# Performance work log

Hardware: AMD Instinct MI355X
Metric: run time of the kernel (lower is better)

The kernel has to match this reference:

```python
import jax, jax.numpy as jnp
import numpy as np

N = 50000
E = 800000
G = 64  # number of graphs in each batch
IN_DIM = 128
HID = 64
NEG_SLOPE = 0.2


def _glorot(key, shape):
    fan = shape[0] + shape[-1] if len(shape) == 2 else int(np.prod(shape[1:])) + shape[-1]
    lim = float(np.sqrt(6.0 / fan))
    return jax.random.uniform(key, shape, jnp.float32, -lim, lim)


def setup_inputs() -> dict:
    key = jax.random.key(0)
    ks = jax.random.split(key, 16)
    x1 = jax.random.normal(ks[0], (N, IN_DIM), jnp.float32)
    x2 = jax.random.normal(ks[1], (N, IN_DIM), jnp.float32)
    edge_index1 = jax.random.randint(ks[2], (2, E), 0, N, jnp.int64)
    edge_index2 = jax.random.randint(ks[3], (2, E), 0, N, jnp.int64)
    batch1 = jnp.sort(jax.random.randint(ks[4], (N,), 0, G, jnp.int64))
    batch2 = jnp.sort(jax.random.randint(ks[5], (N,), 0, G, jnp.int64))
    # conv1: GATConv(IN_DIM, HID, heads=4)
    W1 = _glorot(ks[6], (IN_DIM, 4 * HID))
    a_src1 = _glorot(ks[7], (1, 4, HID))
    a_dst1 = _glorot(ks[8], (1, 4, HID))
    b1 = jnp.zeros((4 * HID,), jnp.float32)
    # conv2: GATConv(4*HID, HID, heads=1)
    W2 = _glorot(ks[9], (4 * HID, HID))
    a_src2 = _glorot(ks[10], (1, 1, HID))
    a_dst2 = _glorot(ks[11], (1, 1, HID))
    b2 = jnp.zeros((HID,), jnp.float32)
    return {"x1": x1, "edge_index1": edge_index1, "batch1": batch1,
            "x2": x2, "edge_index2": edge_index2, "batch2": batch2,
            "W1": W1, "a_src1": a_src1, "a_dst1": a_dst1, "b1": b1,
            "W2": W2, "a_src2": a_src2, "a_dst2": a_dst2, "b2": b2}


def gat_conv(x, src, dst, W, a_src, a_dst, b, n_nodes, heads, out_dim):
    """PyG GATConv with add_self_loops=True, negative_slope=0.2, concat=True."""
    h = (x @ W).reshape(n_nodes, heads, out_dim)            # [N,H,D]
    alpha_s = jnp.sum(h * a_src, axis=-1)                   # [N,H]
    alpha_d = jnp.sum(h * a_dst, axis=-1)                   # [N,H]
    e = alpha_s[src] + alpha_d[dst]                         # [E',H]
    e = jax.nn.leaky_relu(e, NEG_SLOPE)
    # segment softmax over incoming edges of each destination node
    e_max = jax.ops.segment_max(e, dst, num_segments=n_nodes)
    ex = jnp.exp(e - e_max[dst])
    denom = jax.ops.segment_sum(ex, dst, num_segments=n_nodes)
    alpha = ex / (denom[dst] + 1e-16)                       # [E',H]
    msg = h[src] * alpha[:, :, None]                        # [E',H,D]
    out = jax.ops.segment_sum(msg, dst, num_segments=n_nodes)
    return out.reshape(n_nodes, heads * out_dim) + b


def embed(x, edge_index, batch, W1, a_src1, a_dst1, b1, W2, a_src2, a_dst2, b2):
    loops = jnp.arange(N, dtype=edge_index.dtype)
    src = jnp.concatenate([edge_index[0], loops])
    dst = jnp.concatenate([edge_index[1], loops])
    h = jax.nn.elu(gat_conv(x, src, dst, W1, a_src1, a_dst1, b1, N, 4, HID))
    h = jax.nn.elu(gat_conv(h, src, dst, W2, a_src2, a_dst2, b2, N, 1, HID))
    # global_mean_pool over graph ids
    sums = jax.ops.segment_sum(h, batch, num_segments=G)
    cnt = jax.ops.segment_sum(jnp.ones((N,), h.dtype), batch, num_segments=G)
    return sums / jnp.maximum(cnt, 1.0)[:, None]


def reference(x1, edge_index1, batch1, x2, edge_index2, batch2,
              W1, a_src1, a_dst1, b1, W2, a_src2, a_dst2, b2):
    emb1 = embed(x1, edge_index1, batch1, W1, a_src1, a_dst1, b1, W2, a_src2, a_dst2, b2)
    emb2 = embed(x2, edge_index2, batch2, W1, a_src1, a_dst1, b1, W2, a_src2, a_dst2, b2)
    return (emb1, emb2)
```

## Files before the change

### kernel.cpp

```cpp
#include <hip/hip_runtime.h>
#include <cstdint>
#include <cstddef>

#define NNODES 50000
#define NEDGES 800000
#define NGR    64
#define INDIM  128
#define HIDD   64

typedef __attribute__((ext_vector_type(8))) _Float16 f16x8;
typedef __attribute__((ext_vector_type(2))) _Float16 half2v;
typedef __attribute__((ext_vector_type(4))) float f32x4;

__device__ __forceinline__ float lrelu(float x) { return x > 0.f ? x : 0.2f * x; }
__device__ __forceinline__ float eluf(float x)  { return x > 0.f ? x : expm1f(x); }
__device__ __forceinline__ unsigned short f2h(float x) {
    _Float16 h = (_Float16)x;
    return __builtin_bit_cast(unsigned short, h);
}
__device__ __forceinline__ float h2lo(unsigned int u) {
    half2v h = __builtin_bit_cast(half2v, u);
    return (float)h.x;
}
__device__ __forceinline__ float h2hi(unsigned int u) {
    half2v h = __builtin_bit_cast(half2v, u);
    return (float)h.y;
}

__device__ __forceinline__ void acc8(uint4 u, float we, float* a) {
    a[0] = fmaf(h2lo(u.x), we, a[0]); a[1] = fmaf(h2hi(u.x), we, a[1]);
    a[2] = fmaf(h2lo(u.y), we, a[2]); a[3] = fmaf(h2hi(u.y), we, a[3]);
    a[4] = fmaf(h2lo(u.z), we, a[4]); a[5] = fmaf(h2hi(u.z), we, a[5]);
    a[6] = fmaf(h2lo(u.w), we, a[6]); a[7] = fmaf(h2hi(u.w), we, a[7]);
}

__global__ void cvt_f2h(const float* __restrict__ in, unsigned short* __restrict__ out, int n4) {
    int i = blockIdx.x * 256 + threadIdx.x;
    if (i < n4) {
        float4 v = ((const float4*)in)[i];
        ushort4 o;
        o.x = f2h(v.x); o.y = f2h(v.y); o.z = f2h(v.z); o.w = f2h(v.w);
        ((ushort4*)out)[i] = o;
    }
}

__global__ void count_dst(const int* __restrict__ ei0, const int* __restrict__ ei1,
                          int* __restrict__ cnt, int E, int N) {
    const int* ei = blockIdx.y ? ei1 : ei0;
    int* c = cnt + blockIdx.y * N;
    int e = blockIdx.x * 256 + threadIdx.x;
    if (e < E) atomicAdd(&c[ei[E + e]], 1);
}

__global__ __launch_bounds__(256) void scan_part(const int* __restrict__ cnt,
                                                 int* __restrict__ psum, int n) {
    __shared__ int ws[4];
    const int* c = cnt + blockIdx.y * n;
    int* p = psum + blockIdx.y * 256;
    int lane = threadIdx.x & 63, w = threadIdx.x >> 6;
    int i = blockIdx.x * 256 + threadIdx.x;
    int v = (i < n) ? c[i] : 0;
    #pragma unroll
    for (int off = 32; off >= 1; off >>= 1) v += __shfl_xor(v, off, 64);
    if (lane == 0) ws[w] = v;
    __syncthreads();
    if (threadIdx.x == 0) p[blockIdx.x] = ws[0] + ws[1] + ws[2] + ws[3];
}

__global__ __launch_bounds__(256) void scan_tops(int* __restrict__ psum,
                                                 int* __restrict__ rp, int nb, int n) {
    __shared__ int wsum[4];
    int* p = psum + blockIdx.x * 256;
    int* r = rp + blockIdx.x * (n + 1);
    int tid = threadIdx.x, lane = tid & 63, w = tid >> 6;
    int v = (tid < nb) ? p[tid] : 0;
    int x = v;
    #pragma unroll
    for (int off = 1; off < 64; off <<= 1) {
        int t = __shfl_up(x, off, 64);
        if (lane >= off) x += t;
    }
    if (lane == 63) wsum[w] = x;
    __syncthreads();
    int add = 0;
    for (int k = 0; k < w; k++) add += wsum[k];
    int incl = x + add;
    if (tid < nb) p[tid] = incl - v;
    if (tid == nb - 1) r[n] = incl;
}

__global__ __launch_bounds__(256) void scan_fin(const int* __restrict__ cnt,
                                                const int* __restrict__ psum,
                                                int* __restrict__ rp, int n) {
    __shared__ int wsum[4];
    const int* c = cnt + blockIdx.y * n;
    const int* p = psum + blockIdx.y * 256;
    int* r = rp + blockIdx.y * (n + 1);
    int tid = threadIdx.x, lane = tid & 63, w = tid >> 6;
    int i = blockIdx.x * 256 + tid;
    int v = (i < n) ? c[i] : 0;
    int x = v;
    #pragma unroll
    for (int off = 1; off < 64; off <<= 1) {
        int t = __shfl_up(x, off, 64);
        if (lane >= off) x += t;
    }
    if (lane == 63) wsum[w] = x;
    __syncthreads();
    int add = p[blockIdx.x];
    for (int k = 0; k < w; k++) add += wsum[k];
    if (i < n) r[i] = x + add - v;
}

__global__ void fill_csr(const int* __restrict__ ei0, const int* __restrict__ ei1,
                         const int* __restrict__ rp, int* __restrict__ fc,
                         int* __restrict__ col, int E, int N) {
    int g = blockIdx.y;
    const int* ei = g ? ei1 : ei0;
    const int* r = rp + g * (N + 1);
    int* f = fc + g * N;
    int* cl = col + (size_t)g * E;
    int e = blockIdx.x * 256 + threadIdx.x;
    if (e < E) {
        int s = ei[e];
        int d = ei[E + e];
        int pos = atomicAdd(&f[d], 1);
        cl[r[d] + pos] = s;
    }
}

template<int BN, int WM, int WN, bool AF32>
__global__ __launch_bounds__(256) void gemm_mfma(const void* __restrict__ A0,
                                                 const void* __restrict__ A1,
                                                 size_t Ags,
                                                 const unsigned short* __restrict__ Bw,
                                                 unsigned short* __restrict__ C,
                                                 size_t Cgs,
                                                 int M, int K, int N,
                                                 const float* __restrict__ a_src,
                                                 const float* __restrict__ a_dst,
                                                 float* __restrict__ as_o,
                                                 float* __restrict__ ad_o,
                                                 int hstride, int ags) {
    constexpr int BM = 128, BK = 64;
    constexpr int MI = WM / 16, NI = WN / 16;
    constexpr int LDA = BK + 8;
    __shared__ unsigned short Asm[BM * LDA];
    __shared__ unsigned short Bsm[BN * LDA];
    int gph = blockIdx.z;
    const float* Af = (const float*)(gph ? A1 : A0);
    const unsigned short* Ab = (const unsigned short*)A0 + (size_t)gph * Ags;
    unsigned short* Cg = C + (size_t)gph * Cgs;
    float* aso = as_o + (size_t)gph * ags;
    float* ado = ad_o + (size_t)gph * ags;
    int tid = threadIdx.x;
    int lane = tid & 63, wave = tid >> 6;
    int l15 = lane & 15, quad = lane >> 4;
    int wm0, wn0;
    if (BN == 128) { wm0 = (wave >> 1) * 64; wn0 = (wave & 1) * 64; }
    else           { wm0 = wave * 32;        wn0 = 0; }
    int row0 = blockIdx.x * BM;
    int c0 = blockIdx.y * BN;

    f32x4 acc[MI][NI];
    #pragma unroll
    for (int mi = 0; mi < MI; mi++)
        #pragma unroll
        for (int ni = 0; ni < NI; ni++)
            acc[mi][ni] = (f32x4){0.f, 0.f, 0.f, 0.f};

    for (int k0 = 0; k0 < K; k0 += BK) {
        #pragma unroll
        for (int q = 0; q < BM / 32; q++) {
            int idx = q * 256 + tid;
            int r = idx >> 3, kc = idx & 7;
            int row = row0 + r;
            if (AF32) {
                float4 v0 = make_float4(0.f, 0.f, 0.f, 0.f), v1 = v0;
                if (row < M) {
                    v0 = *(const float4*)(Af + (size_t)row * K + k0 + kc * 8);
                    v1 = *(const float4*)(Af + (size_t)row * K + k0 + kc * 8 + 4);
                }
                unsigned short t[8] = {f2h(v0.x), f2h(v0.y), f2h(v0.z), f2h(v0.w),
                                       f2h(v1.x), f2h(v1.y), f2h(v1.z), f2h(v1.w)};
                *(uint4*)&Asm[r * LDA + kc * 8] = *(uint4*)t;
            } else {
                uint4 v = make_uint4(0u, 0u, 0u, 0u);
                if (row < M) v = *(const uint4*)(Ab + (size_t)row * K + k0 + kc * 8);
                *(uint4*)&Asm[r * LDA + kc * 8] = v;
            }
        }
        #pragma unroll
        for (int q = 0; q < BN / 32; q++) {
            int idx = q * 256 + tid;
            int n  = idx & (BN - 1);
            int kc = idx / BN;
            unsigned short tmp[8];
            #pragma unroll
            for (int j = 0; j < 8; j++)
                tmp[j] = Bw[(size_t)(k0 + kc * 8 + j) * N + c0 + n];
            *(uint4*)&Bsm[n * LDA + kc * 8] = *(uint4*)tmp;
        }
        __syncthreads();
        #pragma unroll
        for (int kb = 0; kb < 2; kb++) {
            f16x8 af[MI], bfr[NI];
            #pragma unroll
            for (int mi = 0; mi < MI; mi++)
                af[mi] = *(f16x8*)&Asm[(wm0 + mi * 16 + l15) * LDA + kb * 32 + quad * 8];
            #pragma unroll
            for (int ni = 0; ni < NI; ni++)
                bfr[ni] = *(f16x8*)&Bsm[(wn0 + ni * 16 + l15) * LDA + kb * 32 + quad * 8];
            #pragma unroll
            for (int mi = 0; mi < MI; mi++)
                #pragma unroll
                for (int ni = 0; ni < NI; ni++)
                    acc[mi][ni] = __builtin_amdgcn_mfma_f32_16x16x32_f16(
                        af[mi], bfr[ni], acc[mi][ni], 0, 0, 0);
        }
        __syncthreads();
    }
    #pragma unroll
    for (int mi = 0; mi < MI; mi++) {
        #pragma unroll
        for (int r = 0; r < 4; r++) {
            int row = row0 + wm0 + mi * 16 + quad * 4 + r;
            if (row < M) {
                #pragma unroll
                for (int ni = 0; ni < NI; ni++) {
                    int colg = c0 + wn0 + ni * 16 + l15;
                    Cg[(size_t)row * N + colg] = f2h(acc[mi][ni][r]);
                }
            }
        }
    }
    int headc = (c0 + wn0) >> 6;
    float a_s[NI], a_d[NI];
    #pragma unroll
    for (int ni = 0; ni < NI; ni++) {
        a_s[ni] = a_src[headc * 64 + ni * 16 + l15];
        a_d[ni] = a_dst[headc * 64 + ni * 16 + l15];
    }
    #pragma unroll
    for (int mi = 0; mi < MI; mi++) {
        #pragma unroll
        for (int r = 0; r < 4; r++) {
            float ps = 0.f, pd = 0.f;
            #pragma unroll
            for (int ni = 0; ni < NI; ni++) {
                ps += acc[mi][ni][r] * a_s[ni];
                pd += acc[mi][ni][r] * a_d[ni];
            }
            #pragma unroll
            for (int off = 1; off < 16; off <<= 1) {
                ps += __shfl_xor(ps, off, 64);
                pd += __shfl_xor(pd, off, 64);
            }
            int row = row0 + wm0 + mi * 16 + quad * 4 + r;
            if (l15 == 0 && row < M) {
                aso[row * hstride + headc] = ps;
                ado[row * hstride + headc] = pd;
            }
        }
    }
}

__global__ __launch_bounds__(256) void agg_h4(const unsigned short* __restrict__ h,
                                              size_t hgs,
                                              const float* __restrict__ as_,
                                              const float* __restrict__ ad_, int ags,
                                              const int* __restrict__ rp,
                                              const int* __restrict__ col,
                                              const float* __restrict__ bias,
                                              unsigned short* __restrict__ out,
                                              size_t ogs, int n, int E) {
    int gph = blockIdx.y;
    const uint4* h4 = (const uint4*)(h + (size_t)gph * hgs);
    const float* as = as_ + (size_t)gph * ags;
    const float* adp = ad_ + (size_t)gph * ags;
    const int* r = rp + gph * (n + 1);
    const int* cl = col + (size_t)gph * E;
    unsigned short* og = out + (size_t)gph * ogs;

    int wave = threadIdx.x >> 6, lane = threadIdx.x & 63;
    int node = blockIdx.x * 4 + wave;
    if (node >= n) return;
    int p = lane >> 4;
    int c = lane & 15;
    int headc = c >> 2;
    float adv_q = adp[node * 4 + p];
    float w0 = __expf(lrelu(as[node * 4 + headc] + adp[node * 4 + headc]));
    float m0 = (p == 0) ? w0 : 0.f;
    uint4 hu0 = h4[(size_t)node * 32 + 2 * c];
    uint4 hu1 = h4[(size_t)node * 32 + 2 * c + 1];
    float den = m0;
    float a[16] = {0.f, 0.f, 0.f, 0.f, 0.f, 0.f, 0.f, 0.f,
                   0.f, 0.f, 0.f, 0.f, 0.f, 0.f, 0.f, 0.f};
    acc8(hu0, m0, a);
    acc8(hu1, m0, a + 8);
    int beg = __builtin_amdgcn_readfirstlane(r[node]);
    int end = __builtin_amdgcn_readfirstlane(r[node + 1]);
    int hbase = headc << 4;
    int j = beg;
    int m = end - j; if (m > 16) m = 16;
    int colv = 0; float asv = 0.f;
    if (j < end) {
        colv = cl[j + (c < m ? c : m - 1)];
        asv = as[colv * 4 + p];
    }
    while (j < end) {
        int jn = j + 16;
        int mn = end - jn; if (mn > 16) mn = 16;
        int colv_n = 0; float asv_n = 0.f;
        if (mn > 0) {
            colv_n = cl[jn + (c < mn ? c : mn - 1)];
            asv_n = as[colv_n * 4 + p];
        }
        float wl = __expf(lrelu(asv + adv_q));
        int e0 = p;
        int ec = e0 < m ? e0 : m - 1;
        float we = __shfl(wl, hbase | ec);
        if (e0 >= m) we = 0.f;
        int s = __shfl(colv, ec);
        uint4 u0 = h4[(size_t)s * 32 + 2 * c];
        uint4 u1 = h4[(size_t)s * 32 + 2 * c + 1];
        for (int base = 4; base < m; base += 4) {
            int e2 = base + p;
            int ec2 = e2 < m ? e2 : m - 1;
            float we2 = __shfl(wl, hbase | ec2);
            if (e2 >= m) we2 = 0.f;
            int s2 = __shfl(colv, ec2);
            uint4 v0 = h4[(size_t)s2 * 32 + 2 * c];
            uint4 v1 = h4[(size_t)s2 * 32 + 2 * c + 1];
            den += we;
            acc8(u0, we, a);
            acc8(u1, we, a + 8);
            we = we2; u0 = v0; u1 = v1;
        }
        den += we;
        acc8(u0, we, a);
        acc8(u1, we, a + 8);
        j = jn; m = mn; colv = colv_n; asv = asv_n;
    }
    #pragma unroll
    for (int off = 16; off < 64; off <<= 1) {
        den += __shfl_xor(den, off);
        #pragma unroll
        for (int k = 0; k < 16; k++) a[k] += __shfl_xor(a[k], off);
    }
    if (p == 0) {
        float rden = 1.f / (den + 1e-16f);
        const float4* b4 = (const float4*)bias;
        unsigned short t[16];
        #pragma unroll
        for (int q = 0; q < 4; q++) {
            float4 bq = b4[c * 4 + q];
            t[4 * q]     = f2h(eluf(a[4 * q]     * rden + bq.x));
            t[4 * q + 1] = f2h(eluf(a[4 * q + 1] * rden + bq.y));
            t[4 * q + 2] = f2h(eluf(a[4 * q + 2] * rden + bq.z));
            t[4 * q + 3] = f2h(eluf(a[4 * q + 3] * rden + bq.w));
        }
        uint4* orow = (uint4*)(og + (size_t)node * 256);
        orow[2 * c]     = *(uint4*)&t[0];
        orow[2 * c + 1] = *(uint4*)&t[8];
    }
}

__global__ __launch_bounds__(256) void agg_h1(const unsigned short* __restrict__ h,
                                              size_t hgs,
                                              const float* __restrict__ as_,
                                              const float* __restrict__ ad_,
                                              const int* __restrict__ rp,
                                              const int* __restrict__ col,
                                              const float* __restrict__ bias,
                                              float* __restrict__ out,
                                              size_t ogs, int n, int E) {
    int gph = blockIdx.y;
    const uint4* h4 = (const uint4*)(h + (size_t)gph * hgs);
    const float* as = as_ + (size_t)gph * n;
    const float* adp = ad_ + (size_t)gph * n;
    const int* r = rp + gph * (n + 1);
    const int* cl = col + (size_t)gph * E;
    float* og = out + (size_t)gph * ogs;

    int wave = threadIdx.x >> 6, lane = threadIdx.x & 63;
    int node = blockIdx.x * 4 + wave;
    if (node >= n) return;
    int p = lane >> 3;
    int c = lane & 7;
    float adv = adp[node];
    float w0 = __expf(lrelu(as[node] + adv));
    float m0 = (p == 0) ? w0 : 0.f;
    uint4 hu = h4[(size_t)node * 8 + c];
    float den = m0;
    float a[8] = {0.f, 0.f, 0.f, 0.f, 0.f, 0.f, 0.f, 0.f};
    acc8(hu, m0, a);
    int beg = __builtin_amdgcn_readfirstlane(r[node]);
    int end = __builtin_amdgcn_readfirstlane(r[node + 1]);
    int j = beg;
    int m = end - j; if (m > 64) m = 64;
    int colv = 0; float asv = 0.f;
    if (j < end) {
        colv = cl[j + (lane < m ? lane : m - 1)];
        asv = as[colv];
    }
    while (j < end) {
        int jn = j + 64;
        int mn = end - jn; if (mn > 64) mn = 64;
        int colv_n = 0; float asv_n = 0.f;
        if (mn > 0) {
            colv_n = cl[jn + (lane < mn ? lane : mn - 1)];
            asv_n = as[colv_n];
        }
        float wl = __expf(lrelu(asv + adv));
        int e0 = p;
        int ec = e0 < m ? e0 : m - 1;
        float we = __shfl(wl, ec);
        if (e0 >= m) we = 0.f;
        int s = __shfl(colv, ec);
        uint4 u = h4[(size_t)s * 8 + c];
        for (int base = 8; base < m; base += 8) {
            int e2 = base + p;
            int ec2 = e2 < m ? e2 : m - 1;
            float we2 = __shfl(wl, ec2);
            if (e2 >= m) we2 = 0.f;
            int s2 = __shfl(colv, ec2);
            uint4 u2 = h4[(size_t)s2 * 8 + c];
            den += we;
            acc8(u, we, a);
            we = we2; u = u2;
        }
        den += we;
        acc8(u, we, a);
        j = jn; m = mn; colv = colv_n; asv = asv_n;
    }
    #pragma unroll
    for (int off = 8; off < 64; off <<= 1) {
        den += __shfl_xor(den, off);
        #pragma unroll
        for (int k = 0; k < 8; k++) a[k] += __shfl_xor(a[k], off);
    }
    if (p == 0) {
        float rden = 1.f / (den + 1e-16f);
        float4 b0 = ((const float4*)bias)[c * 2];
        float4 b1 = ((const float4*)bias)[c * 2 + 1];
        float4 o0, o1;
        o0.x = eluf(a[0] * rden + b0.x); o0.y = eluf(a[1] * rden + b0.y);
        o0.z = eluf(a[2] * rden + b0.z); o0.w = eluf(a[3] * rden + b0.w);
        o1.x = eluf(a[4] * rden + b1.x); o1.y = eluf(a[5] * rden + b1.y);
        o1.z = eluf(a[6] * rden + b1.z); o1.w = eluf(a[7] * rden + b1.w);
        float* orow = og + (size_t)node * 64 + c * 8;
        *(float4*)orow = o0;
        *(float4*)(orow + 4) = o1;
    }
}

__device__ __forceinline__ int lbound(const int* __restrict__ a, int n, int key) {
    int lo = 0, hi = n;
    while (lo < hi) {
        int mid = (lo + hi) >> 1;
        if (a[mid] < key) lo = mid + 1; else hi = mid;
    }
    return lo;
}

__global__ __launch_bounds__(256) void pool_mean(const float* __restrict__ g2,
                                                 size_t ggs,
                                                 const int* __restrict__ b0,
                                                 const int* __restrict__ b1,
                                                 float* __restrict__ out, int n) {
    __shared__ float red[4][64];
    __shared__ int bnds[2];
    int gph = blockIdx.y;
    const int* batch = gph ? b1 : b0;
    const float* gg = g2 + (size_t)gph * ggs;
    float* og = out + (size_t)gph * NGR * HIDD;
    int g = blockIdx.x;
    if (threadIdx.x < 2) bnds[threadIdx.x] = lbound(batch, n, g + (int)threadIdx.x);
    __syncthreads();
    int s = bnds[0], e = bnds[1];
    int lane = threadIdx.x & 63, wave = threadIdx.x >> 6;
    float acc = 0.f;
    for (int i = s + wave; i < e; i += 4)
        acc += gg[(size_t)i * 64 + lane];
    red[wave][lane] = acc;
    __syncthreads();
    if (wave == 0) {
        float sum = red[0][lane] + red[1][lane] + red[2][lane] + red[3][lane];
        og[g * 64 + lane] = sum / fmaxf((float)(e - s), 1.0f);
    }
}

extern "C" void kernel_launch(void* const* d_in, const int* in_sizes, int n_in,
                              void* d_out, int out_size, void* d_ws, size_t ws_size,
                              hipStream_t stream) {
    const int N = NNODES, E = NEDGES;

    const float* x1 = (const float*)d_in[0];
    const float* x2 = (const float*)d_in[3];
    const int* ei1v = (const int*)d_in[1];
    const int* ei2v = (const int*)d_in[4];
    const int* ba1  = (const int*)d_in[2];
    const int* ba2  = (const int*)d_in[5];
    const float* W1     = (const float*)d_in[6];
    const float* a_src1 = (const float*)d_in[7];
    const float* a_dst1 = (const float*)d_in[8];
    const float* b1     = (const float*)d_in[9];
    const float* W2     = (const float*)d_in[10];
    const float* a_src2 = (const float*)d_in[11];
    const float* a_dst2 = (const float*)d_in[12];
    const float* b2     = (const float*)d_in[13];

    char* ws = (char*)d_ws;
    size_t off = 0;
    auto carve = [&](size_t bytes) -> char* {
        char* p = ws + off;
        off = (off + bytes + 255) & ~(size_t)255;
        return p;
    };
    char* R1 = carve((size_t)2 * N * 256 * 2);
    char* R2 = carve((size_t)2 * N * 256 * 2);
    char* R3 = carve((size_t)2 * N * 64 * 2);
    int*   col  = (int*)carve((size_t)2 * E * 4);
    int*   rp   = (int*)carve((size_t)2 * (N + 1) * 4);
    int*   cntN = (int*)carve((size_t)2 * N * 4);
    int*   psum = (int*)carve(2 * 256 * 4);
    float* as1  = (float*)carve((size_t)2 * N * 4 * 4);
    float* ad1  = (float*)carve((size_t)2 * N * 4 * 4);
    float* as2  = (float*)carve((size_t)2 * N * 4);
    float* ad2  = (float*)carve((size_t)2 * N * 4);
    unsigned short* W1h = (unsigned short*)carve(INDIM * 256 * 2);
    unsigned short* W2h = (unsigned short*)carve(256 * HIDD * 2);

    unsigned short* h1 = (unsigned short*)R1;
    unsigned short* g1 = (unsigned short*)R2;
    unsigned short* h2 = (unsigned short*)R3;
    float* g2 = (float*)R1;

    float* outF = (float*)d_out;

    const int nodeBlocks = (N + 3) / 4;
    const int nb = (N + 255) / 256;
    const int eb = (E + 255) / 256;

    cvt_f2h<<<(INDIM * 256 / 4 + 255) / 256, 256, 0, stream>>>(W1, W1h, INDIM * 256 / 4);
    cvt_f2h<<<(256 * HIDD / 4 + 255) / 256, 256, 0, stream>>>(W2, W2h, 256 * HIDD / 4);

    hipMemsetAsync(cntN, 0, (size_t)2 * N * 4, stream);
    count_dst<<<dim3(eb, 2), 256, 0, stream>>>(ei1v, ei2v, cntN, E, N);
    scan_part<<<dim3(nb, 2), 256, 0, stream>>>(cntN, psum, N);
    scan_tops<<<2, 256, 0, stream>>>(psum, rp, nb, N);
    scan_fin<<<dim3(nb, 2), 256, 0, stream>>>(cntN, psum, rp, N);
    hipMemsetAsync(cntN, 0, (size_t)2 * N * 4, stream);
    fill_csr<<<dim3(eb, 2), 256, 0, stream>>>(ei1v, ei2v, rp, cntN, col, E, N);

    gemm_mfma<128, 64, 64, true><<<dim3(391, 2, 2), 256, 0, stream>>>(
        x1, x2, 0, W1h, h1, (size_t)N * 256, N, INDIM, 256,
        a_src1, a_dst1, as1, ad1, 4, N * 4);
    agg_h4<<<dim3(nodeBlocks, 2), 256, 0, stream>>>(h1, (size_t)N * 256, as1, ad1, N * 4,
                                                    rp, col, b1, g1, (size_t)N * 256, N, E);

    gemm_mfma<64, 32, 64, false><<<dim3(391, 1, 2), 256, 0, stream>>>(
        g1, nullptr, (size_t)N * 256, W2h, h2, (size_t)N * 64, N, 256, HIDD,
        a_src2, a_dst2, as2, ad2, 1, N);
    agg_h1<<<dim3(nodeBlocks, 2), 256, 0, stream>>>(h2, (size_t)N * 64, as2, ad2,
                                                    rp, col, b2, g2, (size_t)N * 64, N, E);

    pool_mean<<<dim3(NGR, 2), 256, 0, stream>>>(g2, (size_t)N * 64, ba1, ba2, outF, N);
}
```

Baseline: 573.4 us.

## Precompute normalized attention weights, then aggregate with one lane per feature chunk

Splits each GAT aggregation into a weight-prep kernel and an aggregation kernel. The prep kernel computes the softmax-normalized edge weights and stores them as fp16 per edge. The aggregation kernel then walks edges sequentially, with each lane owning a slice of features, so the cross-lane reductions and shuffles of the old version are gone. The cost is two extra kernel launches, a second pass over the edges in prep (exp is computed twice), extra traffic to write and read alpha, and a reuse of the R3 buffer for both alpha1 and h2, which is only safe because of stream ordering.

```diff
diff --git a/kernel.cpp b/kernel.cpp
--- a/kernel.cpp
+++ b/kernel.cpp
@@ -18,6 +18,9 @@
     _Float16 h = (_Float16)x;
     return __builtin_bit_cast(unsigned short, h);
 }
+__device__ __forceinline__ float h2f(unsigned short u) {
+    return (float)__builtin_bit_cast(_Float16, u);
+}
 __device__ __forceinline__ float h2lo(unsigned int u) {
     half2v h = __builtin_bit_cast(half2v, u);
     return (float)h.x;
@@ -25,13 +28,6 @@
 __device__ __forceinline__ float h2hi(unsigned int u) {
     half2v h = __builtin_bit_cast(half2v, u);
     return (float)h.y;
-}
-
-__device__ __forceinline__ void acc8(uint4 u, float we, float* a) {
-    a[0] = fmaf(h2lo(u.x), we, a[0]); a[1] = fmaf(h2hi(u.x), we, a[1]);
-    a[2] = fmaf(h2lo(u.y), we, a[2]); a[3] = fmaf(h2hi(u.y), we, a[3]);
-    a[4] = fmaf(h2lo(u.z), we, a[4]); a[5] = fmaf(h2hi(u.z), we, a[5]);
-    a[6] = fmaf(h2lo(u.w), we, a[6]); a[7] = fmaf(h2hi(u.w), we, a[7]);
 }
 
 __global__ void cvt_f2h(const float* __restrict__ in, unsigned short* __restrict__ out, int n4) {
@@ -265,194 +261,209 @@
     }
 }
 
-__global__ __launch_bounds__(256) void agg_h4(const unsigned short* __restrict__ h,
-                                              size_t hgs,
-                                              const float* __restrict__ as_,
-                                              const float* __restrict__ ad_, int ags,
+__global__ __launch_bounds__(256) void wprep4(const float* __restrict__ as_,
+                                              const float* __restrict__ ad_,
                                               const int* __restrict__ rp,
                                               const int* __restrict__ col,
-                                              const float* __restrict__ bias,
-                                              unsigned short* __restrict__ out,
-                                              size_t ogs, int n, int E) {
+                                              unsigned short* __restrict__ alpha,
+                                              float* __restrict__ alpha0,
+                                              int n, int E) {
     int gph = blockIdx.y;
-    const uint4* h4 = (const uint4*)(h + (size_t)gph * hgs);
-    const float* as = as_ + (size_t)gph * ags;
-    const float* adp = ad_ + (size_t)gph * ags;
+    const float* as = as_ + (size_t)gph * n * 4;
+    const float* ad = ad_ + (size_t)gph * n * 4;
+    const int* r = rp + gph * (n + 1);
+    const int* cl = col + (size_t)gph * E;
+    unsigned short* al = alpha + (size_t)gph * E * 4;
+    float* al0 = alpha0 + (size_t)gph * n * 4;
+
+    int wave = threadIdx.x >> 6, lane = threadIdx.x & 63;
+    int node = blockIdx.x * 4 + wave;
+    if (node >= n) return;
+    int h = lane >> 4, i = lane & 15;
+    float adn = ad[node * 4 + h];
+    float asn = as[node * 4 + h];
+    float w0 = __expf(lrelu(asn + adn));
+    int beg = __builtin_amdgcn_readfirstlane(r[node]);
+    int end = __builtin_amdgcn_readfirstlane(r[node + 1]);
+    float den = 0.f;
+    for (int j = beg; j < end; j += 16) {
+        int idx = j + i;
+        bool v = idx < end;
+        int ix = v ? idx : beg;
+        int colv = cl[ix];
+        float w = __expf(lrelu(as[colv * 4 + h] + adn));
+        den += v ? w : 0.f;
+    }
+    #pragma unroll
+    for (int off = 1; off < 16; off <<= 1) den += __shfl_xor(den, off, 64);
+    den += w0;
+    float rden = 1.f / (den + 1e-16f);
+    for (int j = beg; j < end; j += 16) {
+        int idx = j + i;
+        bool v = idx < end;
+        int ix = v ? idx : beg;
+        int colv = cl[ix];
+        float w = __expf(lrelu(as[colv * 4 + h] + adn));
+        if (v) al[(size_t)idx * 4 + h] = f2h(w * rden);
+    }
+    if (i == 0) al0[node * 4 + h] = w0 * rden;
+}
+
+__global__ __launch_bounds__(256) void wprep1(const float* __restrict__ as_,
+                                              const float* __restrict__ ad_,
+                                              const int* __restrict__ rp,
+                                              const int* __restrict__ col,
+                                              unsigned short* __restrict__ alpha,
+                                              float* __restrict__ alpha0,
+                                              int n, int E) {
+    int gph = blockIdx.y;
+    const float* as = as_ + (size_t)gph * n;
+    const float* ad = ad_ + (size_t)gph * n;
+    const int* r = rp + gph * (n + 1);
+    const int* cl = col + (size_t)gph * E;
+    unsigned short* al = alpha + (size_t)gph * E;
+    float* al0 = alpha0 + (size_t)gph * n;
+
+    int wave = threadIdx.x >> 6, lane = threadIdx.x & 63;
+    int node = blockIdx.x * 4 + wave;
+    if (node >= n) return;
+    float adn = ad[node];
+    float w0 = __expf(lrelu(as[node] + adn));
+    int beg = __builtin_amdgcn_readfirstlane(r[node]);
+    int end = __builtin_amdgcn_readfirstlane(r[node + 1]);
+    float den = 0.f;
+    for (int j = beg; j < end; j += 64) {
+        int idx = j + lane;
+        bool v = idx < end;
+        int ix = v ? idx : beg;
+        int colv = cl[ix];
+        float w = __expf(lrelu(as[colv] + adn));
+        den += v ? w : 0.f;
+    }
+    #pragma unroll
+    for (int off = 1; off < 64; off <<= 1) den += __shfl_xor(den, off, 64);
+    den += w0;
+    float rden = 1.f / (den + 1e-16f);
+    for (int j = beg; j < end; j += 64) {
+        int idx = j + lane;
+        bool v = idx < end;
+        int ix = v ? idx : beg;
+        int colv = cl[ix];
+        float w = __expf(lrelu(as[colv] + adn));
+        if (v) al[idx] = f2h(w * rden);
+    }
+    if (lane == 0) al0[node] = w0 * rden;
+}
+
+__global__ __launch_bounds__(256) void agg4_seq(const unsigned short* __restrict__ h,
+                                                size_t hgs,
+                                                const unsigned short* __restrict__ alpha,
+                                                const float* __restrict__ alpha0,
+                                                const int* __restrict__ rp,
+                                                const int* __restrict__ col,
+                                                const float* __restrict__ bias,
+                                                unsigned short* __restrict__ out,
+                                                size_t ogs, int n, int E) {
+    int gph = blockIdx.y;
+    const unsigned short* hg = h + (size_t)gph * hgs;
+    const unsigned short* al = alpha + (size_t)gph * E * 4;
+    const float* al0 = alpha0 + (size_t)gph * n * 4;
     const int* r = rp + gph * (n + 1);
     const int* cl = col + (size_t)gph * E;
     unsigned short* og = out + (size_t)gph * ogs;
 
-    int wave = threadIdx.x >> 6, lane = threadIdx.x & 63;
+    int wave = threadIdx.x >> 6, c = threadIdx.x & 63;
     int node = blockIdx.x * 4 + wave;
     if (node >= n) return;
-    int p = lane >> 4;
-    int c = lane & 15;
-    int headc = c >> 2;
-    float adv_q = adp[node * 4 + p];
-    float w0 = __expf(lrelu(as[node * 4 + headc] + adp[node * 4 + headc]));
-    float m0 = (p == 0) ? w0 : 0.f;
-    uint4 hu0 = h4[(size_t)node * 32 + 2 * c];
-    uint4 hu1 = h4[(size_t)node * 32 + 2 * c + 1];
-    float den = m0;
-    float a[16] = {0.f, 0.f, 0.f, 0.f, 0.f, 0.f, 0.f, 0.f,
-                   0.f, 0.f, 0.f, 0.f, 0.f, 0.f, 0.f, 0.f};
-    acc8(hu0, m0, a);
-    acc8(hu1, m0, a + 8);
+    int head = c >> 4;
+
+    float a0w = al0[node * 4 + head];
+    uint2 hu = *(const uint2*)(hg + (size_t)node * 256 + c * 4);
+    float a[4];
+    a[0] = h2lo(hu.x) * a0w; a[1] = h2hi(hu.x) * a0w;
+    a[2] = h2lo(hu.y) * a0w; a[3] = h2hi(hu.y) * a0w;
+
     int beg = __builtin_amdgcn_readfirstlane(r[node]);
     int end = __builtin_amdgcn_readfirstlane(r[node + 1]);
-    int hbase = headc << 4;
-    int j = beg;
-    int m = end - j; if (m > 16) m = 16;
-    int colv = 0; float asv = 0.f;
-    if (j < end) {
-        colv = cl[j + (c < m ? c : m - 1)];
-        asv = as[colv * 4 + p];
-    }
-    while (j < end) {
-        int jn = j + 16;
-        int mn = end - jn; if (mn > 16) mn = 16;
-        int colv_n = 0; float asv_n = 0.f;
-        if (mn > 0) {
-            colv_n = cl[jn + (c < mn ? c : mn - 1)];
-            asv_n = as[colv_n * 4 + p];
-        }
-        float wl = __expf(lrelu(asv + adv_q));
-        int e0 = p;
-        int ec = e0 < m ? e0 : m - 1;
-        float we = __shfl(wl, hbase | ec);
-        if (e0 >= m) we = 0.f;
-        int s = __shfl(colv, ec);
-        uint4 u0 = h4[(size_t)s * 32 + 2 * c];
-        uint4 u1 = h4[(size_t)s * 32 + 2 * c + 1];
-        for (int base = 4; base < m; base += 4) {
-            int e2 = base + p;
-            int ec2 = e2 < m ? e2 : m - 1;
-            float we2 = __shfl(wl, hbase | ec2);
-            if (e2 >= m) we2 = 0.f;
-            int s2 = __shfl(colv, ec2);
-            uint4 v0 = h4[(size_t)s2 * 32 + 2 * c];
-            uint4 v1 = h4[(size_t)s2 * 32 + 2 * c + 1];
-            den += we;
-            acc8(u0, we, a);
-            acc8(u1, we, a + 8);
-            we = we2; u0 = v0; u1 = v1;
-        }
-        den += we;
-        acc8(u0, we, a);
-        acc8(u1, we, a + 8);
-        j = jn; m = mn; colv = colv_n; asv = asv_n;
-    }
-    #pragma unroll
-    for (int off = 16; off < 64; off <<= 1) {
-        den += __shfl_xor(den, off);
-        #pragma unroll
-        for (int k = 0; k < 16; k++) a[k] += __shfl_xor(a[k], off);
-    }
-    if (p == 0) {
-        float rden = 1.f / (den + 1e-16f);
-        const float4* b4 = (const float4*)bias;
-        unsigned short t[16];
-        #pragma unroll
-        for (int q = 0; q < 4; q++) {
-            float4 bq = b4[c * 4 + q];
-            t[4 * q]     = f2h(eluf(a[4 * q]     * rden + bq.x));
-            t[4 * q + 1] = f2h(eluf(a[4 * q + 1] * rden + bq.y));
-            t[4 * q + 2] = f2h(eluf(a[4 * q + 2] * rden + bq.z));
-            t[4 * q + 3] = f2h(eluf(a[4 * q + 3] * rden + bq.w));
-        }
-        uint4* orow = (uint4*)(og + (size_t)node * 256);
-        orow[2 * c]     = *(uint4*)&t[0];
-        orow[2 * c + 1] = *(uint4*)&t[8];
-    }
-}
-
-__global__ __launch_bounds__(256) void agg_h1(const unsigned short* __restrict__ h,
-                                              size_t hgs,
-                                              const float* __restrict__ as_,
-                                              const float* __restrict__ ad_,
-                                              const int* __restrict__ rp,
-                                              const int* __restrict__ col,
-                                              const float* __restrict__ bias,
-                                              float* __restrict__ out,
-                                              size_t ogs, int n, int E) {
+    for (int j = beg; j < end; j += 8) {
+        float we[8]; uint2 uu[8];
+        #pragma unroll
+        for (int k = 0; k < 8; k++) {
+            int idx = j + k;
+            bool v = idx < end;
+            int ix = v ? idx : beg;
+            int s = cl[ix];
+            unsigned short aw = al[(size_t)ix * 4 + head];
+            we[k] = v ? h2f(aw) : 0.f;
+            uu[k] = *(const uint2*)(hg + (size_t)s * 256 + c * 4);
+        }
+        #pragma unroll
+        for (int k = 0; k < 8; k++) {
+            a[0] = fmaf(h2lo(uu[k].x), we[k], a[0]);
+            a[1] = fmaf(h2hi(uu[k].x), we[k], a[1]);
+            a[2] = fmaf(h2lo(uu[k].y), we[k], a[2]);
+            a[3] = fmaf(h2hi(uu[k].y), we[k], a[3]);
+        }
+    }
+    float4 bq = ((const float4*)bias)[c];
+    ushort4 t;
+    t.x = f2h(eluf(a[0] + bq.x));
+    t.y = f2h(eluf(a[1] + bq.y));
+    t.z = f2h(eluf(a[2] + bq.z));
+    t.w = f2h(eluf(a[3] + bq.w));
+    *(uint2*)(og + (size_t)node * 256 + c * 4) = *(uint2*)&t;
+}
+
+__global__ __launch_bounds__(256) void agg1_seq(const unsigned short* __restrict__ h,
+                                                size_t hgs,
+                                                const unsigned short* __restrict__ alpha,
+                                                const float* __restrict__ alpha0,
+                                                const int* __restrict__ rp,
+                                                const int* __restrict__ col,
+                                                const float* __restrict__ bias,
+                                                float* __restrict__ out,
+                                                size_t ogs, int n, int E) {
     int gph = blockIdx.y;
-    const uint4* h4 = (const uint4*)(h + (size_t)gph * hgs);
-    const float* as = as_ + (size_t)gph * n;
-    const float* adp = ad_ + (size_t)gph * n;
+    const unsigned short* hg = h + (size_t)gph * hgs;
+    const unsigned short* al = alpha + (size_t)gph * E;
+    const float* al0 = alpha0 + (size_t)gph * n;
     const int* r = rp + gph * (n + 1);
     const int* cl = col + (size_t)gph * E;
     float* og = out + (size_t)gph * ogs;
 
     int wave = threadIdx.x >> 6, lane = threadIdx.x & 63;
-    int node = blockIdx.x * 4 + wave;
+    int p = lane >> 5, c = lane & 31;
+    int node = blockIdx.x * 8 + wave * 2 + p;
     if (node >= n) return;
-    int p = lane >> 3;
-    int c = lane & 7;
-    float adv = adp[node];
-    float w0 = __expf(lrelu(as[node] + adv));
-    float m0 = (p == 0) ? w0 : 0.f;
-    uint4 hu = h4[(size_t)node * 8 + c];
-    float den = m0;
-    float a[8] = {0.f, 0.f, 0.f, 0.f, 0.f, 0.f, 0.f, 0.f};
-    acc8(hu, m0, a);
-    int beg = __builtin_amdgcn_readfirstlane(r[node]);
-    int end = __builtin_amdgcn_readfirstlane(r[node + 1]);
-    int j = beg;
-    int m = end - j; if (m > 64) m = 64;
-    int colv = 0; float asv = 0.f;
-    if (j < end) {
-        colv = cl[j + (lane < m ? lane : m - 1)];
-        asv = as[colv];
-    }
-    while (j < end) {
-        int jn = j + 64;
-        int mn = end - jn; if (mn > 64) mn = 64;
-        int colv_n = 0; float asv_n = 0.f;
-        if (mn > 0) {
-            colv_n = cl[jn + (lane < mn ? lane : mn - 1)];
-            asv_n = as[colv_n];
-        }
-        float wl = __expf(lrelu(asv + adv));
-        int e0 = p;
-        int ec = e0 < m ? e0 : m - 1;
-        float we = __shfl(wl, ec);
-        if (e0 >= m) we = 0.f;
-        int s = __shfl(colv, ec);
-        uint4 u = h4[(size_t)s * 8 + c];
-        for (int base = 8; base < m; base += 8) {
-            int e2 = base + p;
-            int ec2 = e2 < m ? e2 : m - 1;
-            float we2 = __shfl(wl, ec2);
-            if (e2 >= m) we2 = 0.f;
-            int s2 = __shfl(colv, ec2);
-            uint4 u2 = h4[(size_t)s2 * 8 + c];
-            den += we;
-            acc8(u, we, a);
-            we = we2; u = u2;
-        }
-        den += we;
-        acc8(u, we, a);
-        j = jn; m = mn; colv = colv_n; asv = asv_n;
-    }
-    #pragma unroll
-    for (int off = 8; off < 64; off <<= 1) {
-        den += __shfl_xor(den, off);
-        #pragma unroll
-        for (int k = 0; k < 8; k++) a[k] += __shfl_xor(a[k], off);
-    }
-    if (p == 0) {
-        float rden = 1.f / (den + 1e-16f);
-        float4 b0 = ((const float4*)bias)[c * 2];
-        float4 b1 = ((const float4*)bias)[c * 2 + 1];
-        float4 o0, o1;
-        o0.x = eluf(a[0] * rden + b0.x); o0.y = eluf(a[1] * rden + b0.y);
-        o0.z = eluf(a[2] * rden + b0.z); o0.w = eluf(a[3] * rden + b0.w);
-        o1.x = eluf(a[4] * rden + b1.x); o1.y = eluf(a[5] * rden + b1.y);
-        o1.z = eluf(a[6] * rden + b1.z); o1.w = eluf(a[7] * rden + b1.w);
-        float* orow = og + (size_t)node * 64 + c * 8;
-        *(float4*)orow = o0;
-        *(float4*)(orow + 4) = o1;
-    }
+
+    float a0w = al0[node];
+    unsigned int hu = *(const unsigned int*)(hg + (size_t)node * 64 + c * 2);
+    float a0 = h2lo(hu) * a0w, a1 = h2hi(hu) * a0w;
+
+    int beg = r[node], end = r[node + 1];
+    for (int j = beg; j < end; j += 8) {
+        float we[8]; unsigned int uu[8];
+        #pragma unroll
+        for (int k = 0; k < 8; k++) {
+            int idx = j + k;
+            bool v = idx < end;
+            int ix = v ? idx : beg;
+            int s = cl[ix];
+            unsigned short aw = al[ix];
+            we[k] = v ? h2f(aw) : 0.f;
+            uu[k] = *(const unsigned int*)(hg + (size_t)s * 64 + c * 2);
+        }
+        #pragma unroll
+        for (int k = 0; k < 8; k++) {
+            a0 = fmaf(h2lo(uu[k]), we[k], a0);
+            a1 = fmaf(h2hi(uu[k]), we[k], a1);
+        }
+    }
+    float2 bq = ((const float2*)bias)[c];
+    float2 o;
+    o.x = eluf(a0 + bq.x);
+    o.y = eluf(a1 + bq.y);
+    *(float2*)(og + (size_t)node * 64 + c * 2) = o;
 }
 
 __device__ __forceinline__ int lbound(const int* __restrict__ a, int n, int key) {
@@ -520,7 +531,7 @@
     };
     char* R1 = carve((size_t)2 * N * 256 * 2);
     char* R2 = carve((size_t)2 * N * 256 * 2);
-    char* R3 = carve((size_t)2 * N * 64 * 2);
+    char* R3 = carve((size_t)2 * E * 4 * 2);
     int*   col  = (int*)carve((size_t)2 * E * 4);
     int*   rp   = (int*)carve((size_t)2 * (N + 1) * 4);
     int*   cntN = (int*)carve((size_t)2 * N * 4);
@@ -529,11 +540,15 @@
     float* ad1  = (float*)carve((size_t)2 * N * 4 * 4);
     float* as2  = (float*)carve((size_t)2 * N * 4);
     float* ad2  = (float*)carve((size_t)2 * N * 4);
+    float* al01 = (float*)carve((size_t)2 * N * 4 * 4);
+    float* al02 = (float*)carve((size_t)2 * N * 4);
+    unsigned short* alpha2 = (unsigned short*)carve((size_t)2 * E * 2);
     unsigned short* W1h = (unsigned short*)carve(INDIM * 256 * 2);
     unsigned short* W2h = (unsigned short*)carve(256 * HIDD * 2);
 
     unsigned short* h1 = (unsigned short*)R1;
     unsigned short* g1 = (unsigned short*)R2;
+    unsigned short* alpha1 = (unsigned short*)R3;
     unsigned short* h2 = (unsigned short*)R3;
     float* g2 = (float*)R1;
 
@@ -557,14 +572,16 @@
     gemm_mfma<128, 64, 64, true><<<dim3(391, 2, 2), 256, 0, stream>>>(
         x1, x2, 0, W1h, h1, (size_t)N * 256, N, INDIM, 256,
         a_src1, a_dst1, as1, ad1, 4, N * 4);
-    agg_h4<<<dim3(nodeBlocks, 2), 256, 0, stream>>>(h1, (size_t)N * 256, as1, ad1, N * 4,
-                                                    rp, col, b1, g1, (size_t)N * 256, N, E);
+    wprep4<<<dim3(nodeBlocks, 2), 256, 0, stream>>>(as1, ad1, rp, col, alpha1, al01, N, E);
+    agg4_seq<<<dim3(nodeBlocks, 2), 256, 0, stream>>>(h1, (size_t)N * 256, alpha1, al01,
+                                                      rp, col, b1, g1, (size_t)N * 256, N, E);
 
     gemm_mfma<64, 32, 64, false><<<dim3(391, 1, 2), 256, 0, stream>>>(
         g1, nullptr, (size_t)N * 256, W2h, h2, (size_t)N * 64, N, 256, HIDD,
         a_src2, a_dst2, as2, ad2, 1, N);
-    agg_h1<<<dim3(nodeBlocks, 2), 256, 0, stream>>>(h2, (size_t)N * 64, as2, ad2,
-                                                    rp, col, b2, g2, (size_t)N * 64, N, E);
+    wprep1<<<dim3(nodeBlocks, 2), 256, 0, stream>>>(as2, ad2, rp, col, alpha2, al02, N, E);
+    agg1_seq<<<dim3((N + 7) / 8, 2), 256, 0, stream>>>(h2, (size_t)N * 64, alpha2, al02,
+                                                       rp, col, b2, g2, (size_t)N * 64, N, E);
 
     pool_mean<<<dim3(NGR, 2), 256, 0, stream>>>(g2, (size_t)N * 64, ba1, ba2, outF, N);
 }
```

Result: slower. 648.7 us (+13.1%).
